# Kernel tuning notes

Measured on AMD Instinct MI355X. Metric: run time of the kernel, lower is better.

Reference implementation:

```python
import jax, jax.numpy as jnp
import numpy as np

N1D = 64   # 1D LUT knots per channel
M3D = 17   # 3D LUT grid size per axis
B, H, W = 4, 1024, 1024


def setup_inputs() -> dict:
    key = jax.random.key(0)
    kx, k1, k3 = jax.random.split(key, 3)
    x = jax.random.uniform(kx, (B, 3, H, W), dtype=jnp.float32)
    # learned LUTs: identity transform + small perturbation (realistic trained state)
    ramp = jnp.linspace(0.0, 1.0, N1D, dtype=jnp.float32)
    lut1d = jnp.tile(ramp[None, :], (3, 1)) + 0.02 * jax.random.normal(k1, (3, N1D), dtype=jnp.float32)
    g = jnp.linspace(0.0, 1.0, M3D, dtype=jnp.float32)
    rr, gg, bb = jnp.meshgrid(g, g, g, indexing='ij')
    lut3d = jnp.stack([rr, gg, bb], axis=-1) + 0.02 * jax.random.normal(k3, (M3D, M3D, M3D, 3), dtype=jnp.float32)
    return {"x": x, "lut1d": lut1d, "lut3d": lut3d}


def _apply_lut1d(x, lut1d):
    # x: [B,3,H,W] in [0,1]; lut1d: [3,N] per-channel curve, linear interp
    n = lut1d.shape[1]
    xs = x * (n - 1)
    i0 = jnp.clip(jnp.floor(xs).astype(jnp.int32), 0, n - 2)
    f = xs - i0.astype(x.dtype)
    v0 = jnp.stack([jnp.take(lut1d[c], i0[:, c]) for c in range(3)], axis=1)
    v1 = jnp.stack([jnp.take(lut1d[c], i0[:, c] + 1) for c in range(3)], axis=1)
    return v0 + f * (v1 - v0)


def _apply_lut3d(x, lut3d):
    # x: [B,3,H,W] in [0,1]; lut3d: [M,M,M,3] -> trilinear interpolation
    m = lut3d.shape[0]
    xs = x * (m - 1)
    i0 = jnp.clip(jnp.floor(xs).astype(jnp.int32), 0, m - 2)
    f = xs - i0.astype(x.dtype)
    ir, ig, ib = i0[:, 0], i0[:, 1], i0[:, 2]          # each [B,H,W]
    fr = f[:, 0, :, :, None]                            # [B,H,W,1]
    fg = f[:, 1, :, :, None]
    fb = f[:, 2, :, :, None]
    flat = lut3d.reshape(m * m * m, 3)

    def corner(dr, dg, db):
        lin = ((ir + dr) * m + (ig + dg)) * m + (ib + db)
        return flat[lin]                                # gather -> [B,H,W,3]

    out = (corner(0, 0, 0) * (1 - fr) * (1 - fg) * (1 - fb)
           + corner(1, 0, 0) * fr * (1 - fg) * (1 - fb)
           + corner(0, 1, 0) * (1 - fr) * fg * (1 - fb)
           + corner(0, 0, 1) * (1 - fr) * (1 - fg) * fb
           + corner(1, 1, 0) * fr * fg * (1 - fb)
           + corner(1, 0, 1) * fr * (1 - fg) * fb
           + corner(0, 1, 1) * (1 - fr) * fg * fb
           + corner(1, 1, 1) * fr * fg * fb)
    return jnp.moveaxis(out, -1, 1)                     # [B,3,H,W]


def reference(x, lut1d, lut3d):
    y = _apply_lut1d(x, lut1d)
    y = jnp.clip(y, 0.0, 1.0)
    return _apply_lut3d(y, lut3d)
```

## Files before the change

kernel.cpp:

```cpp
#include <hip/hip_runtime.h>
#include <hip/hip_fp16.h>

constexpr int kHW = 1024 * 1024;
constexpr int kChunksPerImage = kHW / 4;
constexpr int kM3 = 17 * 17 * 17;

constexpr int kBlock = 512;
constexpr int kGrid  = 2048;

__device__ __forceinline__ float h2f_lo(unsigned int u) {
    __half2 h = *reinterpret_cast<__half2*>(&u);
    return __low2float(h);
}

__device__ __forceinline__ float apply1d(const float2* __restrict__ s1, int c, float v) {
    float xs = v * 63.0f;
    int i0 = (int)xs;
    i0 = min(max(i0, 0), 62);
    float f = xs - (float)i0;
    float2 p = s1[(c << 6) + i0];
    return fmaf(f, p.y - p.x, p.x);
}

struct F3 { float x, y, z; };

__device__ __forceinline__ F3 tri3d(const uint2* __restrict__ s3,
                                    float yr, float yg, float yb) {
    float xr = yr * 16.0f, xg = yg * 16.0f, xb = yb * 16.0f;
    int ir = min((int)xr, 15);
    int ig = min((int)xg, 15);
    int ib = min((int)xb, 15);
    float fr = xr - (float)ir;
    float fg = xg - (float)ig;
    float fb = xb - (float)ib;

    const int cell = (ir * 17 + ig) * 17 + ib;

    auto blerp = [&](const uint2* __restrict__ p) -> F3 {
        uint2 e0 = p[0];
        uint2 e1 = p[1];
        float2 a01 = __half22float2(*reinterpret_cast<__half2*>(&e0.x));
        float  a2  = h2f_lo(e0.y);
        float2 b01 = __half22float2(*reinterpret_cast<__half2*>(&e1.x));
        float  b2  = h2f_lo(e1.y);
        F3 r;
        r.x = fmaf(fb, b01.x - a01.x, a01.x);
        r.y = fmaf(fb, b01.y - a01.y, a01.y);
        r.z = fmaf(fb, b2 - a2, a2);
        return r;
    };

    F3 v00 = blerp(s3 + cell);
    F3 v01 = blerp(s3 + cell + 17);
    F3 v10 = blerp(s3 + cell + 289);
    F3 v11 = blerp(s3 + cell + 306);

    F3 v0, v1, vf;
    v0.x = fmaf(fg, v01.x - v00.x, v00.x);
    v0.y = fmaf(fg, v01.y - v00.y, v00.y);
    v0.z = fmaf(fg, v01.z - v00.z, v00.z);
    v1.x = fmaf(fg, v11.x - v10.x, v10.x);
    v1.y = fmaf(fg, v11.y - v10.y, v10.y);
    v1.z = fmaf(fg, v11.z - v10.z, v10.z);
    vf.x = fmaf(fr, v1.x - v0.x, v0.x);
    vf.y = fmaf(fr, v1.y - v0.y, v0.y);
    vf.z = fmaf(fr, v1.z - v0.z, v0.z);
    return vf;
}

__global__ __launch_bounds__(kBlock) void lut_apply_kernel(
    const float* __restrict__ x,
    const float* __restrict__ lut1d,
    const float* __restrict__ lut3d,
    float* __restrict__ out)
{
    __shared__ uint2  s3[kM3];
    __shared__ float2 s1[3 * 64];

    for (int i = threadIdx.x; i < kM3; i += kBlock) {
        float c0 = lut3d[3 * i], c1 = lut3d[3 * i + 1], c2 = lut3d[3 * i + 2];
        __half2 h01 = __floats2half2_rn(c0, c1);
        __half2 h2p = __floats2half2_rn(c2, 0.0f);
        uint2 e;
        e.x = *reinterpret_cast<unsigned int*>(&h01);
        e.y = *reinterpret_cast<unsigned int*>(&h2p);
        s3[i] = e;
    }
    for (int i = threadIdx.x; i < 3 * 64; i += kBlock) {
        int c = i >> 6, j = i & 63;
        float a = lut1d[(c << 6) + j];
        float b = lut1d[(c << 6) + (j < 63 ? j + 1 : 63)];
        s1[i] = make_float2(a, b);
    }
    __syncthreads();

    const int q   = blockIdx.x * kBlock + threadIdx.x;
    const int b   = q >> 18;
    const int rem = q & (kChunksPerImage - 1);
    const size_t base = (size_t)(3 * b) * kHW + 4 * (size_t)rem;

    const float4 r4 = *(const float4*)(x + base);
    const float4 g4 = *(const float4*)(x + base + kHW);
    const float4 b4 = *(const float4*)(x + base + 2 * kHW);

    const float rin[4] = {r4.x, r4.y, r4.z, r4.w};
    const float gin[4] = {g4.x, g4.y, g4.z, g4.w};
    const float bin[4] = {b4.x, b4.y, b4.z, b4.w};
    float ro[4], go[4], bo[4];

    #pragma unroll
    for (int k = 0; k < 4; ++k) {
        float yr = apply1d(s1, 0, rin[k]);
        float yg = apply1d(s1, 1, gin[k]);
        float yb = apply1d(s1, 2, bin[k]);
        yr = fminf(fmaxf(yr, 0.0f), 1.0f);
        yg = fminf(fmaxf(yg, 0.0f), 1.0f);
        yb = fminf(fmaxf(yb, 0.0f), 1.0f);

        F3 v = tri3d(s3, yr, yg, yb);
        ro[k] = v.x; go[k] = v.y; bo[k] = v.z;
    }

    *(float4*)(out + base)           = make_float4(ro[0], ro[1], ro[2], ro[3]);
    *(float4*)(out + base + kHW)     = make_float4(go[0], go[1], go[2], go[3]);
    *(float4*)(out + base + 2 * kHW) = make_float4(bo[0], bo[1], bo[2], bo[3]);
}

extern "C" void kernel_launch(void* const* d_in, const int* in_sizes, int n_in,
                              void* d_out, int out_size, void* d_ws, size_t ws_size,
                              hipStream_t stream) {
    const float* x     = (const float*)d_in[0];
    const float* lut1d = (const float*)d_in[1];
    const float* lut3d = (const float*)d_in[2];
    float* out = (float*)d_out;

    hipLaunchKernelGGL(lut_apply_kernel, dim3(kGrid), dim3(kBlock), 0, stream,
                       x, lut1d, lut3d, out);
}
```

Measured before the change: 114.8 us.

## Prepack LUTs in separate kernel, split 3D LUT planes, use bpermute for 1D LUT

Adds a small pre-pass kernel that packs both LUTs into fp16 pairs in workspace, so each main-kernel block only does a vectorised uint4 copy into LDS instead of converting the LUTs itself. The 3D LUT is stored as two planes: (r,g) pairs, and (b, next b) pairs. Each corner then needs three 32-bit LDS reads instead of two 64-bit ones. The 1D LUT lives in registers and is read with ds_bpermute across lanes rather than LDS. This trades an extra kernel launch and lower 1D LUT precision (fp16 instead of fp32) for less per-block setup and fewer LDS bytes per lookup.

```diff
diff --git a/kernel.cpp b/kernel.cpp
--- a/kernel.cpp
+++ b/kernel.cpp
@@ -5,26 +5,59 @@
 constexpr int kChunksPerImage = kHW / 4;
 constexpr int kM3 = 17 * 17 * 17;
 
+constexpr int kPA   = 4928;
+constexpr int kLdsU = 2 * kPA;
+constexpr int kP1   = kLdsU;
+
 constexpr int kBlock = 512;
 constexpr int kGrid  = 2048;
 
-__device__ __forceinline__ float h2f_lo(unsigned int u) {
-    __half2 h = *reinterpret_cast<__half2*>(&u);
-    return __low2float(h);
+__device__ __forceinline__ float2 h2f2(unsigned int u) {
+    return __half22float2(*reinterpret_cast<__half2*>(&u));
+}
+__device__ __forceinline__ unsigned int packh2(float a, float b) {
+    __half2 h = __floats2half2_rn(a, b);
+    return *reinterpret_cast<unsigned int*>(&h);
 }
 
-__device__ __forceinline__ float apply1d(const float2* __restrict__ s1, int c, float v) {
+__global__ void pack_kernel(const float* __restrict__ lut1d,
+                            const float* __restrict__ lut3d,
+                            unsigned int* __restrict__ ws) {
+    const int i = blockIdx.x * 256 + threadIdx.x;
+    if (i < kPA) {
+        unsigned int a = 0, b = 0;
+        if (i < kM3) {
+            float c0 = lut3d[3 * i], c1 = lut3d[3 * i + 1], c2 = lut3d[3 * i + 2];
+            int j = (i + 1 < kM3) ? i + 1 : i;
+            float c2n = lut3d[3 * j + 2];
+            a = packh2(c0, c1);
+            b = packh2(c2, c2n);
+        }
+        ws[i]       = a;
+        ws[kPA + i] = b;
+    }
+    if (i < 192) {
+        int c = i >> 6, j = i & 63;
+        float l0 = lut1d[(c << 6) + j];
+        float l1 = lut1d[(c << 6) + (j < 63 ? j + 1 : 63)];
+        ws[kP1 + i] = packh2(l0, l1);
+    }
+}
+
+__device__ __forceinline__ float apply1d_bp(unsigned int treg, float v) {
     float xs = v * 63.0f;
-    int i0 = (int)xs;
-    i0 = min(max(i0, 0), 62);
+    int i0 = min(max((int)xs, 0), 62);
     float f = xs - (float)i0;
-    float2 p = s1[(c << 6) + i0];
+    unsigned int pair =
+        (unsigned int)__builtin_amdgcn_ds_bpermute(i0 << 2, (int)treg);
+    float2 p = h2f2(pair);
     return fmaf(f, p.y - p.x, p.x);
 }
 
 struct F3 { float x, y, z; };
 
-__device__ __forceinline__ F3 tri3d(const uint2* __restrict__ s3,
+__device__ __forceinline__ F3 tri3d(const unsigned int* __restrict__ sA,
+                                    const unsigned int* __restrict__ sB,
                                     float yr, float yg, float yb) {
     float xr = yr * 16.0f, xg = yg * 16.0f, xb = yb * 16.0f;
     int ir = min((int)xr, 15);
@@ -36,24 +69,22 @@
 
     const int cell = (ir * 17 + ig) * 17 + ib;
 
-    auto blerp = [&](const uint2* __restrict__ p) -> F3 {
-        uint2 e0 = p[0];
-        uint2 e1 = p[1];
-        float2 a01 = __half22float2(*reinterpret_cast<__half2*>(&e0.x));
-        float  a2  = h2f_lo(e0.y);
-        float2 b01 = __half22float2(*reinterpret_cast<__half2*>(&e1.x));
-        float  b2  = h2f_lo(e1.y);
+    auto corner = [&](int c) -> F3 {
+        unsigned int a0 = sA[c];
+        unsigned int a1 = sA[c + 1];
+        unsigned int bp = sB[c];
+        float2 A0 = h2f2(a0), A1 = h2f2(a1), Bc = h2f2(bp);
         F3 r;
-        r.x = fmaf(fb, b01.x - a01.x, a01.x);
-        r.y = fmaf(fb, b01.y - a01.y, a01.y);
-        r.z = fmaf(fb, b2 - a2, a2);
+        r.x = fmaf(fb, A1.x - A0.x, A0.x);
+        r.y = fmaf(fb, A1.y - A0.y, A0.y);
+        r.z = fmaf(fb, Bc.y - Bc.x, Bc.x);
         return r;
     };
 
-    F3 v00 = blerp(s3 + cell);
-    F3 v01 = blerp(s3 + cell + 17);
-    F3 v10 = blerp(s3 + cell + 289);
-    F3 v11 = blerp(s3 + cell + 306);
+    F3 v00 = corner(cell);
+    F3 v01 = corner(cell + 17);
+    F3 v10 = corner(cell + 289);
+    F3 v11 = corner(cell + 306);
 
     F3 v0, v1, vf;
     v0.x = fmaf(fg, v01.x - v00.x, v00.x);
@@ -70,29 +101,24 @@
 
 __global__ __launch_bounds__(kBlock) void lut_apply_kernel(
     const float* __restrict__ x,
-    const float* __restrict__ lut1d,
-    const float* __restrict__ lut3d,
+    const unsigned int* __restrict__ ws,
     float* __restrict__ out)
 {
-    __shared__ uint2  s3[kM3];
-    __shared__ float2 s1[3 * 64];
+    __shared__ uint4 ldsv[kLdsU / 4];
+    unsigned int* lds = (unsigned int*)ldsv;
 
-    for (int i = threadIdx.x; i < kM3; i += kBlock) {
-        float c0 = lut3d[3 * i], c1 = lut3d[3 * i + 1], c2 = lut3d[3 * i + 2];
-        __half2 h01 = __floats2half2_rn(c0, c1);
-        __half2 h2p = __floats2half2_rn(c2, 0.0f);
-        uint2 e;
-        e.x = *reinterpret_cast<unsigned int*>(&h01);
-        e.y = *reinterpret_cast<unsigned int*>(&h2p);
-        s3[i] = e;
-    }
-    for (int i = threadIdx.x; i < 3 * 64; i += kBlock) {
-        int c = i >> 6, j = i & 63;
-        float a = lut1d[(c << 6) + j];
-        float b = lut1d[(c << 6) + (j < 63 ? j + 1 : 63)];
-        s1[i] = make_float2(a, b);
-    }
+    const uint4* wsv = (const uint4*)ws;
+    #pragma unroll 1
+    for (int i = threadIdx.x; i < kLdsU / 4; i += kBlock) ldsv[i] = wsv[i];
+
+    const int lane = threadIdx.x & 63;
+    const unsigned int t0 = ws[kP1 + lane];
+    const unsigned int t1 = ws[kP1 + 64 + lane];
+    const unsigned int t2 = ws[kP1 + 128 + lane];
     __syncthreads();
+
+    const unsigned int* sA = lds;
+    const unsigned int* sB = lds + kPA;
 
     const int q   = blockIdx.x * kBlock + threadIdx.x;
     const int b   = q >> 18;
@@ -110,14 +136,14 @@
 
     #pragma unroll
     for (int k = 0; k < 4; ++k) {
-        float yr = apply1d(s1, 0, rin[k]);
-        float yg = apply1d(s1, 1, gin[k]);
-        float yb = apply1d(s1, 2, bin[k]);
+        float yr = apply1d_bp(t0, rin[k]);
+        float yg = apply1d_bp(t1, gin[k]);
+        float yb = apply1d_bp(t2, bin[k]);
         yr = fminf(fmaxf(yr, 0.0f), 1.0f);
         yg = fminf(fmaxf(yg, 0.0f), 1.0f);
         yb = fminf(fmaxf(yb, 0.0f), 1.0f);
 
-        F3 v = tri3d(s3, yr, yg, yb);
+        F3 v = tri3d(sA, sB, yr, yg, yb);
         ro[k] = v.x; go[k] = v.y; bo[k] = v.z;
     }
 
@@ -133,7 +159,10 @@
     const float* lut1d = (const float*)d_in[1];
     const float* lut3d = (const float*)d_in[2];
     float* out = (float*)d_out;
+    unsigned int* ws = (unsigned int*)d_ws;
 
+    hipLaunchKernelGGL(pack_kernel, dim3(64), dim3(256), 0, stream,
+                       lut1d, lut3d, ws);
     hipLaunchKernelGGL(lut_apply_kernel, dim3(kGrid), dim3(kBlock), 0, stream,
-                       x, lut1d, lut3d, out);
+                       x, ws, out);
 }
```

Result: faster. 108.7 us (-5.3%).
